# Kernel tuning notes

Measured on AMD Instinct MI355X. Metric: run time of the kernel, lower is better.

The kernel has to match this reference:

```python
import jax, jax.numpy as jnp
import numpy as np

N_TOKENS = 32768
EMBED_DIM = 1024
NUM_EXPERTS = 64
TOP_K = 2


def setup_inputs() -> dict:
    key = jax.random.key(0)
    kx, kw = jax.random.split(key)
    x = jax.random.normal(kx, (N_TOKENS, EMBED_DIM), dtype=jnp.float32)
    # nn.Linear(embed_dim, num_experts).weight has shape (num_experts, embed_dim)
    W_gate = jax.random.normal(kw, (NUM_EXPERTS, EMBED_DIM), dtype=jnp.float32) * 0.02
    return {"x": x, "W_gate": W_gate}


def reference(x, W_gate):
    # (N, E) router logits: x @ W.T
    logits = jnp.einsum("nd,ed->ne", x, W_gate)
    probs = jax.nn.softmax(logits, axis=-1)
    top_k_probs, top_k_indices = jax.lax.top_k(probs, TOP_K)
    top_k_probs = top_k_probs / jnp.sum(top_k_probs, axis=-1, keepdims=True)
    # load-balancing aux loss
    expert_mask = jnp.sum(jax.nn.one_hot(top_k_indices, NUM_EXPERTS, dtype=jnp.float32), axis=1)  # (N, E)
    f = jnp.mean(expert_mask, axis=0)  # fraction of tokens routed to each expert (sums to top_k)
    p = jnp.mean(probs, axis=0)        # mean gate prob per expert
    aux_loss = NUM_EXPERTS * jnp.sum(f * p)
    return (top_k_probs, top_k_indices, aux_loss)
```

## Files before the change

### kernel.cpp

```cpp
#include <hip/hip_runtime.h>
#include <cstdint>

#define N_TOK   32768
#define DIM     1024
#define NEXP    64
#define TM      128
#define BK      32
#define KITERS  (DIM / BK)
#define NTHR    256

typedef uint32_t __attribute__((address_space(3))) lds_u32_t;
typedef const uint32_t __attribute__((address_space(1))) glb_u32_t;

__device__ __forceinline__ void gload16(const float* g, float4* l) {
  __builtin_amdgcn_global_load_lds((glb_u32_t*)g, (lds_u32_t*)l, 16, 0, 0);
}

__device__ __forceinline__ int swz(int r, int s) { return (r << 3) + (s ^ ((r >> 2) & 7)); }

__launch_bounds__(NTHR, 1)
__global__ void router_kernel(const float* __restrict__ x,
                              const float* __restrict__ Wg,
                              float* __restrict__ out,
                              unsigned int* __restrict__ cnt_g,
                              float* __restrict__ sp_g) {
  __shared__ float4 Xs4[2][TM * BK / 4];
  __shared__ float4 Ws4[2][NEXP * BK / 4];
  __shared__ float  L[TM * 65];
  __shared__ float  Linv[TM];
  __shared__ float  colpart[4 * NEXP];
  __shared__ unsigned int cnt_s[NEXP];

  const int tid  = threadIdx.x;
  const int tx   = tid & 15;
  const int ty   = tid >> 4;
  const int tok0 = blockIdx.x * TM;

  if (tid < NEXP) cnt_s[tid] = 0;

  int pA[4], pB[2];
  const float* srcA[4];
  const float* srcB[2];
#pragma unroll
  for (int q = 0; q < 4; ++q) {
    int p = q * 256 + tid;
    pA[q] = p;
    int r = p >> 3, sc = p & 7;
    int s = sc ^ ((r >> 2) & 7);
    srcA[q] = x + (size_t)(tok0 + r) * DIM + s * 4;
  }
#pragma unroll
  for (int q = 0; q < 2; ++q) {
    int p = q * 256 + tid;
    pB[q] = p;
    int r = p >> 3, sc = p & 7;
    int s = sc ^ ((r >> 2) & 7);
    srcB[q] = Wg + (size_t)r * DIM + s * 4;
  }

  float acc[8][4];
#pragma unroll
  for (int i = 0; i < 8; ++i)
#pragma unroll
    for (int j = 0; j < 4; ++j) acc[i][j] = 0.f;

#pragma unroll
  for (int q = 0; q < 4; ++q) { gload16(srcA[q], &Xs4[0][pA[q]]); srcA[q] += BK; }
#pragma unroll
  for (int q = 0; q < 2; ++q) { gload16(srcB[q], &Ws4[0][pB[q]]); srcB[q] += BK; }

  for (int it = 0; it < KITERS; ++it) {
    const int b = it & 1;
    if (it < KITERS - 1) {
#pragma unroll
      for (int q = 0; q < 4; ++q) { gload16(srcA[q], &Xs4[b ^ 1][pA[q]]); srcA[q] += BK; }
#pragma unroll
      for (int q = 0; q < 2; ++q) { gload16(srcB[q], &Ws4[b ^ 1][pB[q]]); srcB[q] += BK; }
      asm volatile("s_waitcnt vmcnt(6)" ::: "memory");
    } else {
      asm volatile("s_waitcnt vmcnt(0)" ::: "memory");
    }
    __builtin_amdgcn_s_barrier();
    asm volatile("" ::: "memory");

#pragma unroll
    for (int dd = 0; dd < BK; dd += 4) {
      const int sidx = dd >> 2;
      float4 wv[4];
#pragma unroll
      for (int j = 0; j < 4; ++j) wv[j] = Ws4[b][swz(tx * 4 + j, sidx)];
#pragma unroll
      for (int i = 0; i < 8; ++i) {
        float4 xv = Xs4[b][swz(ty * 8 + i, sidx)];
#pragma unroll
        for (int j = 0; j < 4; ++j) {
          acc[i][j] = fmaf(xv.x, wv[j].x, acc[i][j]);
          acc[i][j] = fmaf(xv.y, wv[j].y, acc[i][j]);
          acc[i][j] = fmaf(xv.z, wv[j].z, acc[i][j]);
          acc[i][j] = fmaf(xv.w, wv[j].w, acc[i][j]);
        }
      }
    }
    asm volatile("" ::: "memory");
    __builtin_amdgcn_s_barrier();
    asm volatile("" ::: "memory");
  }

#pragma unroll
  for (int i = 0; i < 8; ++i)
#pragma unroll
    for (int j = 0; j < 4; ++j)
      L[(ty * 8 + i) * 65 + tx * 4 + j] = acc[i][j];
  __syncthreads();

  if (tid < TM) {
    const int base = tid * 65;
    float v1 = -1e30f, v2 = -1e30f;
    int i1 = 0, i2 = 0;
    for (int e = 0; e < NEXP; ++e) {
      float v = L[base + e];
      if (v > v1)      { v2 = v1; i2 = i1; v1 = v; i1 = e; }
      else if (v > v2) { v2 = v;  i2 = e; }
    }
    float ssum = 0.f;
    for (int e = 0; e < NEXP; ++e) {
      float p = __expf(L[base + e] - v1);
      ssum += p;
      L[base + e] = p;
    }
    Linv[tid] = 1.f / ssum;

    float e2   = __expf(v2 - v1);
    float invn = 1.f / (1.f + e2);
    const int g = tok0 + tid;
    out[2 * g]     = invn;
    out[2 * g + 1] = e2 * invn;
    out[2 * N_TOK + 2 * g]     = (float)i1;
    out[2 * N_TOK + 2 * g + 1] = (float)i2;
    atomicAdd(&cnt_s[i1], 1u);
    atomicAdd(&cnt_s[i2], 1u);
  }
  __syncthreads();

  {
    const int e = tid & 63;
    const int q = tid >> 6;
    float s = 0.f;
#pragma unroll 4
    for (int t = 0; t < 32; ++t) {
      int row = q * 32 + t;
      s += L[row * 65 + e] * Linv[row];
    }
    colpart[q * 64 + e] = s;
  }
  __syncthreads();
  if (tid < NEXP) {
    float tot = colpart[tid] + colpart[64 + tid] + colpart[128 + tid] + colpart[192 + tid];
    atomicAdd(&sp_g[tid], tot);
    atomicAdd(&cnt_g[tid], cnt_s[tid]);
  }
}

__global__ void aux_kernel(const unsigned int* __restrict__ cnt,
                           const float* __restrict__ sp,
                           float* __restrict__ out) {
  const int l = threadIdx.x;
  float v = (float)cnt[l] * sp[l];
#pragma unroll
  for (int off = 32; off > 0; off >>= 1) v += __shfl_down(v, off);
  if (l == 0)
    out[4 * N_TOK] = (float)NEXP * v * (1.f / (float)N_TOK) * (1.f / (float)N_TOK);
}

extern "C" void kernel_launch(void* const* d_in, const int* in_sizes, int n_in,
                              void* d_out, int out_size, void* d_ws, size_t ws_size,
                              hipStream_t stream) {
  const float* x  = (const float*)d_in[0];
  const float* Wg = (const float*)d_in[1];
  float* out = (float*)d_out;
  unsigned int* cnt = (unsigned int*)d_ws;
  float* sp = (float*)((char*)d_ws + 256);

  hipMemsetAsync(d_ws, 0, 512, stream);
  router_kernel<<<dim3(N_TOK / TM), dim3(NTHR), 0, stream>>>(x, Wg, out, cnt, sp);
  aux_kernel<<<dim3(1), dim3(64), 0, stream>>>(cnt, sp, out);
}
```

Before: 255.3 us.

## Rewrite router as per-token register GEMV with split-K waves and fused aux loss

Replaces the LDS-tiled 128x64 GEMM with a design where each thread owns one token and accumulates all 64 expert logits in registers. The four waves split the K dimension and combine their partials through swizzled LDS. Weights are read directly from global memory (cached), and the per-expert sums use shuffles and ballots instead of LDS atomics. The separate aux kernel is dropped in favour of a last-block-done counter, which saves a launch but adds high register pressure and uncoalesced strided x loads per lane.

New measurement: 539.4 us. 2.11x slower.

```diff
diff --git a/kernel.cpp b/kernel.cpp
--- a/kernel.cpp
+++ b/kernel.cpp
@@ -1,175 +1,160 @@
 #include <hip/hip_runtime.h>
 #include <cstdint>
 
-#define N_TOK   32768
-#define DIM     1024
-#define NEXP    64
-#define TM      128
-#define BK      32
-#define KITERS  (DIM / BK)
-#define NTHR    256
+#define N_TOK  32768
+#define DIM    1024
+#define NEXP   64
+#define NTHR   256
+#define TOKB   64
+#define NBLK   (N_TOK / TOKB)
+#define KS     4
+#define KSLICE (DIM / KS)
+#define NCHUNK (KSLICE / 16)
 
-typedef uint32_t __attribute__((address_space(3))) lds_u32_t;
-typedef const uint32_t __attribute__((address_space(1))) glb_u32_t;
-
-__device__ __forceinline__ void gload16(const float* g, float4* l) {
-  __builtin_amdgcn_global_load_lds((glb_u32_t*)g, (lds_u32_t*)l, 16, 0, 0);
-}
-
-__device__ __forceinline__ int swz(int r, int s) { return (r << 3) + (s ^ ((r >> 2) & 7)); }
-
-__launch_bounds__(NTHR, 1)
+__launch_bounds__(NTHR, 2)
 __global__ void router_kernel(const float* __restrict__ x,
                               const float* __restrict__ Wg,
                               float* __restrict__ out,
-                              unsigned int* __restrict__ cnt_g,
-                              float* __restrict__ sp_g) {
-  __shared__ float4 Xs4[2][TM * BK / 4];
-  __shared__ float4 Ws4[2][NEXP * BK / 4];
-  __shared__ float  L[TM * 65];
-  __shared__ float  Linv[TM];
-  __shared__ float  colpart[4 * NEXP];
-  __shared__ unsigned int cnt_s[NEXP];
+                              float* __restrict__ ws) {
+  float* cnt_g = ws;
+  float* sp_g  = ws + 64;
+  unsigned int* done = (unsigned int*)(ws + 128);
+
+  __shared__ float4 cmb[KS][TOKB][16];
+  __shared__ unsigned int lastflag;
 
   const int tid  = threadIdx.x;
-  const int tx   = tid & 15;
-  const int ty   = tid >> 4;
-  const int tok0 = blockIdx.x * TM;
+  const int lane = tid & 63;
+  const int w    = __builtin_amdgcn_readfirstlane(tid >> 6);
+  const int tok  = blockIdx.x * TOKB + lane;
 
-  if (tid < NEXP) cnt_s[tid] = 0;
+  const float4* __restrict__ xr = (const float4*)(x + (size_t)tok * DIM + (size_t)w * KSLICE);
+  const float4* __restrict__ W4 = (const float4*)Wg;
 
-  int pA[4], pB[2];
-  const float* srcA[4];
-  const float* srcB[2];
+  float acc[NEXP];
 #pragma unroll
-  for (int q = 0; q < 4; ++q) {
-    int p = q * 256 + tid;
-    pA[q] = p;
-    int r = p >> 3, sc = p & 7;
-    int s = sc ^ ((r >> 2) & 7);
-    srcA[q] = x + (size_t)(tok0 + r) * DIM + s * 4;
-  }
+  for (int e = 0; e < NEXP; ++e) acc[e] = 0.f;
+
+  auto chunk = [&](const float4* xv, int c) {
 #pragma unroll
-  for (int q = 0; q < 2; ++q) {
-    int p = q * 256 + tid;
-    pB[q] = p;
-    int r = p >> 3, sc = p & 7;
-    int s = sc ^ ((r >> 2) & 7);
-    srcB[q] = Wg + (size_t)r * DIM + s * 4;
-  }
+    for (int e = 0; e < NEXP; e += 2) {
+      const float4* wp0 = W4 + (e * (DIM / 4) + w * (KSLICE / 4) + c * 4);
+      const float4* wp1 = wp0 + (DIM / 4);
+      float4 wa0 = wp0[0], wa1 = wp0[1], wa2 = wp0[2], wa3 = wp0[3];
+      float4 wb0 = wp1[0], wb1 = wp1[1], wb2 = wp1[2], wb3 = wp1[3];
+      float A = acc[e], B = acc[e + 1];
+      A = fmaf(xv[0].x, wa0.x, A); B = fmaf(xv[0].x, wb0.x, B);
+      A = fmaf(xv[0].y, wa0.y, A); B = fmaf(xv[0].y, wb0.y, B);
+      A = fmaf(xv[0].z, wa0.z, A); B = fmaf(xv[0].z, wb0.z, B);
+      A = fmaf(xv[0].w, wa0.w, A); B = fmaf(xv[0].w, wb0.w, B);
+      A = fmaf(xv[1].x, wa1.x, A); B = fmaf(xv[1].x, wb1.x, B);
+      A = fmaf(xv[1].y, wa1.y, A); B = fmaf(xv[1].y, wb1.y, B);
+      A = fmaf(xv[1].z, wa1.z, A); B = fmaf(xv[1].z, wb1.z, B);
+      A = fmaf(xv[1].w, wa1.w, A); B = fmaf(xv[1].w, wb1.w, B);
+      A = fmaf(xv[2].x, wa2.x, A); B = fmaf(xv[2].x, wb2.x, B);
+      A = fmaf(xv[2].y, wa2.y, A); B = fmaf(xv[2].y, wb2.y, B);
+      A = fmaf(xv[2].z, wa2.z, A); B = fmaf(xv[2].z, wb2.z, B);
+      A = fmaf(xv[2].w, wa2.w, A); B = fmaf(xv[2].w, wb2.w, B);
+      A = fmaf(xv[3].x, wa3.x, A); B = fmaf(xv[3].x, wb3.x, B);
+      A = fmaf(xv[3].y, wa3.y, A); B = fmaf(xv[3].y, wb3.y, B);
+      A = fmaf(xv[3].z, wa3.z, A); B = fmaf(xv[3].z, wb3.z, B);
+      A = fmaf(xv[3].w, wa3.w, A); B = fmaf(xv[3].w, wb3.w, B);
+      acc[e] = A; acc[e + 1] = B;
+    }
+  };
 
-  float acc[8][4];
+  float4 xa[4], xb[4];
 #pragma unroll
-  for (int i = 0; i < 8; ++i)
+  for (int q = 0; q < 4; ++q) xa[q] = xr[q];
+
+  for (int c = 0; c < NCHUNK; c += 2) {
 #pragma unroll
-    for (int j = 0; j < 4; ++j) acc[i][j] = 0.f;
-
+    for (int q = 0; q < 4; ++q) xb[q] = xr[(c + 1) * 4 + q];
+    chunk(xa, c);
+    if (c + 2 < NCHUNK) {
 #pragma unroll
-  for (int q = 0; q < 4; ++q) { gload16(srcA[q], &Xs4[0][pA[q]]); srcA[q] += BK; }
-#pragma unroll
-  for (int q = 0; q < 2; ++q) { gload16(srcB[q], &Ws4[0][pB[q]]); srcB[q] += BK; }
-
-  for (int it = 0; it < KITERS; ++it) {
-    const int b = it & 1;
-    if (it < KITERS - 1) {
-#pragma unroll
-      for (int q = 0; q < 4; ++q) { gload16(srcA[q], &Xs4[b ^ 1][pA[q]]); srcA[q] += BK; }
-#pragma unroll
-      for (int q = 0; q < 2; ++q) { gload16(srcB[q], &Ws4[b ^ 1][pB[q]]); srcB[q] += BK; }
-      asm volatile("s_waitcnt vmcnt(6)" ::: "memory");
-    } else {
-      asm volatile("s_waitcnt vmcnt(0)" ::: "memory");
+      for (int q = 0; q < 4; ++q) xa[q] = xr[(c + 2) * 4 + q];
     }
-    __builtin_amdgcn_s_barrier();
-    asm volatile("" ::: "memory");
-
-#pragma unroll
-    for (int dd = 0; dd < BK; dd += 4) {
-      const int sidx = dd >> 2;
-      float4 wv[4];
-#pragma unroll
-      for (int j = 0; j < 4; ++j) wv[j] = Ws4[b][swz(tx * 4 + j, sidx)];
-#pragma unroll
-      for (int i = 0; i < 8; ++i) {
-        float4 xv = Xs4[b][swz(ty * 8 + i, sidx)];
-#pragma unroll
-        for (int j = 0; j < 4; ++j) {
-          acc[i][j] = fmaf(xv.x, wv[j].x, acc[i][j]);
-          acc[i][j] = fmaf(xv.y, wv[j].y, acc[i][j]);
-          acc[i][j] = fmaf(xv.z, wv[j].z, acc[i][j]);
-          acc[i][j] = fmaf(xv.w, wv[j].w, acc[i][j]);
-        }
-      }
-    }
-    asm volatile("" ::: "memory");
-    __builtin_amdgcn_s_barrier();
-    asm volatile("" ::: "memory");
+    chunk(xb, c + 1);
   }
 
 #pragma unroll
-  for (int i = 0; i < 8; ++i)
-#pragma unroll
-    for (int j = 0; j < 4; ++j)
-      L[(ty * 8 + i) * 65 + tx * 4 + j] = acc[i][j];
-  __syncthreads();
-
-  if (tid < TM) {
-    const int base = tid * 65;
-    float v1 = -1e30f, v2 = -1e30f;
-    int i1 = 0, i2 = 0;
-    for (int e = 0; e < NEXP; ++e) {
-      float v = L[base + e];
-      if (v > v1)      { v2 = v1; i2 = i1; v1 = v; i1 = e; }
-      else if (v > v2) { v2 = v;  i2 = e; }
-    }
-    float ssum = 0.f;
-    for (int e = 0; e < NEXP; ++e) {
-      float p = __expf(L[base + e] - v1);
-      ssum += p;
-      L[base + e] = p;
-    }
-    Linv[tid] = 1.f / ssum;
-
-    float e2   = __expf(v2 - v1);
-    float invn = 1.f / (1.f + e2);
-    const int g = tok0 + tid;
-    out[2 * g]     = invn;
-    out[2 * g + 1] = e2 * invn;
-    out[2 * N_TOK + 2 * g]     = (float)i1;
-    out[2 * N_TOK + 2 * g + 1] = (float)i2;
-    atomicAdd(&cnt_s[i1], 1u);
-    atomicAdd(&cnt_s[i2], 1u);
+  for (int q = 0; q < 16; ++q) {
+    float4 v;
+    v.x = acc[4 * q]; v.y = acc[4 * q + 1]; v.z = acc[4 * q + 2]; v.w = acc[4 * q + 3];
+    cmb[w][lane][q ^ (lane & 15)] = v;
   }
   __syncthreads();
 
-  {
-    const int e = tid & 63;
-    const int q = tid >> 6;
-    float s = 0.f;
-#pragma unroll 4
-    for (int t = 0; t < 32; ++t) {
-      int row = q * 32 + t;
-      s += L[row * 65 + e] * Linv[row];
+  if (tid < 64) {
+    float lg[NEXP];
+#pragma unroll
+    for (int q = 0; q < 16; ++q) {
+      const int qs = q ^ (lane & 15);
+      float4 s0 = cmb[0][lane][qs];
+      float4 s1 = cmb[1][lane][qs];
+      float4 s2 = cmb[2][lane][qs];
+      float4 s3 = cmb[3][lane][qs];
+      lg[4 * q]     = s0.x + s1.x + s2.x + s3.x;
+      lg[4 * q + 1] = s0.y + s1.y + s2.y + s3.y;
+      lg[4 * q + 2] = s0.z + s1.z + s2.z + s3.z;
+      lg[4 * q + 3] = s0.w + s1.w + s2.w + s3.w;
     }
-    colpart[q * 64 + e] = s;
+
+    float v1 = lg[0]; int t1 = 0;
+    float v2 = -3.4e38f; int t2 = 0;
+#pragma unroll
+    for (int e = 1; e < NEXP; ++e) {
+      float v = lg[e];
+      if (v > v1)      { v2 = v1; t2 = t1; v1 = v; t1 = e; }
+      else if (v > v2) { v2 = v;  t2 = e; }
+    }
+
+    float ssum = 0.f;
+#pragma unroll
+    for (int e = 0; e < NEXP; ++e) { float p = __expf(lg[e] - v1); lg[e] = p; ssum += p; }
+    const float inv = 1.f / ssum;
+
+    const float e2v = __expf(v2 - v1);
+    const float r   = 1.f / (1.f + e2v);
+    out[2 * tok]     = r;
+    out[2 * tok + 1] = e2v * r;
+    out[2 * N_TOK + 2 * tok]     = (float)t1;
+    out[2 * N_TOK + 2 * tok + 1] = (float)t2;
+
+    float myps = 0.f;
+#pragma unroll
+    for (int e = 0; e < NEXP; ++e) {
+      float s = lg[e] * inv;
+      s += __shfl_xor(s, 1);  s += __shfl_xor(s, 2);  s += __shfl_xor(s, 4);
+      s += __shfl_xor(s, 8);  s += __shfl_xor(s, 16); s += __shfl_xor(s, 32);
+      if (lane == e) myps = s;
+    }
+    float myc = 0.f;
+#pragma unroll
+    for (int e = 0; e < NEXP; ++e) {
+      unsigned long long m1 = __ballot(t1 == e);
+      unsigned long long m2 = __ballot(t2 == e);
+      if (lane == e) myc = (float)(__popcll(m1) + __popcll(m2));
+    }
+    atomicAdd(&sp_g[lane], myps);
+    atomicAdd(&cnt_g[lane], myc);
+  }
+
+  if (tid == 0) {
+    __threadfence();
+    lastflag = (atomicAdd(done, 1u) == NBLK - 1) ? 1u : 0u;
   }
   __syncthreads();
-  if (tid < NEXP) {
-    float tot = colpart[tid] + colpart[64 + tid] + colpart[128 + tid] + colpart[192 + tid];
-    atomicAdd(&sp_g[tid], tot);
-    atomicAdd(&cnt_g[tid], cnt_s[tid]);
+  if (lastflag && tid < 64) {
+    float C = atomicAdd(&cnt_g[lane], 0.f);
+    float S = atomicAdd(&sp_g[lane], 0.f);
+    float v = C * S;
+    v += __shfl_xor(v, 1);  v += __shfl_xor(v, 2);  v += __shfl_xor(v, 4);
+    v += __shfl_xor(v, 8);  v += __shfl_xor(v, 16); v += __shfl_xor(v, 32);
+    if (lane == 0)
+      out[4 * N_TOK] = (float)NEXP * v * (1.f / (float)N_TOK) * (1.f / (float)N_TOK);
   }
-}
-
-__global__ void aux_kernel(const unsigned int* __restrict__ cnt,
-                           const float* __restrict__ sp,
-                           float* __restrict__ out) {
-  const int l = threadIdx.x;
-  float v = (float)cnt[l] * sp[l];
-#pragma unroll
-  for (int off = 32; off > 0; off >>= 1) v += __shfl_down(v, off);
-  if (l == 0)
-    out[4 * N_TOK] = (float)NEXP * v * (1.f / (float)N_TOK) * (1.f / (float)N_TOK);
 }
 
 extern "C" void kernel_launch(void* const* d_in, const int* in_sizes, int n_in,
@@ -178,10 +163,7 @@
   const float* x  = (const float*)d_in[0];
   const float* Wg = (const float*)d_in[1];
   float* out = (float*)d_out;
-  unsigned int* cnt = (unsigned int*)d_ws;
-  float* sp = (float*)((char*)d_ws + 256);
 
-  hipMemsetAsync(d_ws, 0, 512, stream);
-  router_kernel<<<dim3(N_TOK / TM), dim3(NTHR), 0, stream>>>(x, Wg, out, cnt, sp);
-  aux_kernel<<<dim3(1), dim3(64), 0, stream>>>(cnt, sp, out);
+  hipMemsetAsync(d_ws, 0, 1024, stream);
+  router_kernel<<<dim3(NBLK), dim3(NTHR), 0, stream>>>(x, Wg, out, (float*)d_ws);
 }
```
